# Performance work log

Measured on AMD Instinct MI355X. Metric: run time of the kernel, lower is better.

The kernel has to match this reference:

```python
import jax, jax.numpy as jnp
import numpy as np

N_NODES = 100000
N_EDGES = 1600000
H_IN = 128
H_OUT = 128
ELU_ALPHA = 0.1


def setup_inputs() -> dict:
    key = jax.random.key(0)
    k = jax.random.split(key, 6)
    x = jax.random.normal(k[0], (N_NODES, H_IN), dtype=jnp.float32)
    edge_index = jax.random.randint(k[1], (2, N_EDGES), 0, N_NODES, dtype=jnp.int64)
    s = 1.0 / np.sqrt(H_IN)
    W_conv = jax.random.uniform(k[2], (H_IN, H_OUT), jnp.float32, -s, s)
    b_conv = jnp.zeros((H_OUT,), jnp.float32)
    W_skip = jax.random.uniform(k[3], (H_IN, H_OUT), jnp.float32, -s, s)
    b_skip = jax.random.uniform(k[4], (H_OUT,), jnp.float32, -s, s)
    return {"x": x, "edge_index": edge_index, "W_conv": W_conv,
            "b_conv": b_conv, "W_skip": W_skip, "b_skip": b_skip}


def reference(x, edge_index, W_conv, b_conv, W_skip, b_skip):
    # GCNConv(improved=True): add self-loops with weight 2.0, symmetric norm.
    N = x.shape[0]
    src, dst = edge_index[0], edge_index[1]
    # degree = incoming edge weights (1.0 each) + 2.0 self-loop weight
    deg = jnp.zeros((N,), x.dtype).at[dst].add(1.0) + 2.0
    dinv = jax.lax.rsqrt(deg)                     # deg >= 2 always
    norm = dinv[src] * dinv[dst]                  # [E]
    h = x @ W_conv                                # [N, H_OUT]
    # scatter-add of normalized messages over real edges
    agg = jax.ops.segment_sum(norm[:, None] * h[src], dst, num_segments=N)
    # self-loop contribution: weight 2 * dinv[i]^2
    agg = agg + (2.0 * dinv * dinv)[:, None] * h
    out = agg + b_conv + x @ W_skip + b_skip
    # Dropout(p=0.1) in eval mode = identity; ELU(alpha=0.1)
    return jnp.where(out > 0, out, ELU_ALPHA * (jnp.exp(out) - 1.0))
```

## Files before the change

### kernel.cpp

```cpp
#include <hip/hip_runtime.h>
#include <hip/hip_bf16.h>
#include <hip/hip_fp16.h>

#define H 128
#define BW 128
#define BSH 7
#define NB 256
#define TK 32

typedef __attribute__((ext_vector_type(8))) short short8;
typedef __attribute__((ext_vector_type(4))) float f32x4;

__device__ inline unsigned short f2bf(float f) {
    union { float f; unsigned int u; } v; v.f = f;
    unsigned int r = (v.u + 0x7fffu + ((v.u >> 16) & 1u)) >> 16;
    return (unsigned short)r;
}
__device__ inline float bf2f(unsigned short h) {
    union { unsigned int u; float f; } v; v.u = ((unsigned int)h) << 16;
    return v.f;
}

__global__ __launch_bounds__(256) void quant_hist_kernel(const float* __restrict__ x,
                                                         const float* __restrict__ Wc,
                                                         const float* __restrict__ Ws,
                                                         const int* __restrict__ ei,
                                                         uint* __restrict__ xq,
                                                         float* __restrict__ invs,
                                                         short8* __restrict__ wp,
                                                         int* __restrict__ counts,
                                                         int N, int E, int nbu,
                                                         int chunk, int qb) {
    __shared__ int h[1024];
    if (blockIdx.x >= qb) {
        const int b = blockIdx.x - qb;
        for (int i = threadIdx.x; i < nbu; i += 256) h[i] = 0;
        __syncthreads();
        const int lo = b * chunk;
        const int hi = min(E, lo + chunk);
        for (int e = lo + threadIdx.x; e < hi; e += 256)
            atomicAdd(&h[ei[E + e] >> BSH], 1);
        __syncthreads();
        for (int i = threadIdx.x; i < nbu; i += 256) counts[b * nbu + i] = h[i];
        return;
    }
    int node = blockIdx.x * 8 + (threadIdx.x >> 5);
    if (node < N) {
        int l32 = threadIdx.x & 31;
        float4 v = ((const float4*)x)[node * 32 + l32];
        float m = fmaxf(fmaxf(fabsf(v.x), fabsf(v.y)), fmaxf(fabsf(v.z), fabsf(v.w)));
        #pragma unroll
        for (int mk = 1; mk < 32; mk <<= 1) m = fmaxf(m, __shfl_xor(m, mk));
        m = fmaxf(m, 1e-30f);
        float s = 127.0f / m;
        int q0 = min(255, max(0, (int)rintf(v.x * s) + 128));
        int q1 = min(255, max(0, (int)rintf(v.y * s) + 128));
        int q2 = min(255, max(0, (int)rintf(v.z * s) + 128));
        int q3 = min(255, max(0, (int)rintf(v.w * s) + 128));
        xq[node * 32 + l32] = (uint)q0 | ((uint)q1 << 8) | ((uint)q2 << 16) | ((uint)q3 << 24);
        if (l32 == 0) invs[node] = m / 127.0f;
    }
    if (blockIdx.x < 8) {
        int t = blockIdx.x * 256 + threadIdx.x;
        int lane = t & 63;
        int nt = (t >> 6) & 7;
        int ks = t >> 9;
        int kbase = ks * 32 + (lane >> 4) * 8;
        int col = nt * 16 + (lane & 15);
        short8 whc, whs, wls;
        #pragma unroll
        for (int j = 0; j < 8; ++j) {
            float wc = Wc[(kbase + j) * H + col];
            float ws = Ws[(kbase + j) * H + col];
            unsigned short hc = f2bf(wc);
            unsigned short hs = f2bf(ws);
            whc[j] = (short)hc;
            whs[j] = (short)hs;
            wls[j] = (short)f2bf(ws - bf2f(hs));
        }
        int base = (ks * 8 + nt) * 64 + lane;
        wp[base] = whc;
        wp[2048 + base] = whs;
        wp[4096 + base] = wls;
    }
}

__global__ __launch_bounds__(256) void p2_scan(const int* __restrict__ counts,
                                               int* __restrict__ scanned,
                                               int* __restrict__ btot, int nbu) {
    __shared__ int tile[NB][TK + 1];
    __shared__ int segsum[8][TK + 1];
    const int tl = threadIdx.x & 31;
    const int tw = threadIdx.x >> 5;
    const int k = blockIdx.x * TK + tl;
    const bool kok = k < nbu;
    for (int r = tw; r < NB; r += 8)
        tile[r][tl] = kok ? counts[r * nbu + k] : 0;
    __syncthreads();
    const int base = tw * 32;
    int s = 0;
    #pragma unroll
    for (int i = 0; i < 32; ++i) s += tile[base + i][tl];
    segsum[tw][tl] = s;
    __syncthreads();
    int run = 0;
    for (int q = 0; q < tw; ++q) run += segsum[q][tl];
    if (kok) {
        for (int i = 0; i < 32; ++i) {
            int cur = tile[base + i][tl];
            scanned[(base + i) * nbu + k] = run;
            run += cur;
        }
        if (tw == 7) btot[k] = run;
    }
}

__global__ __launch_bounds__(256) void p5_scatter(const int* __restrict__ ei,
                                                  const int* __restrict__ btot,
                                                  const int* __restrict__ scanned,
                                                  int* __restrict__ tmp,
                                                  int* __restrict__ cstart,
                                                  int E, int nbu, int chunk) {
    __shared__ int sc[1024];
    __shared__ int part[256];
    __shared__ int lb[1024];
    const int t = threadIdx.x;
    const int b = blockIdx.x;
    const int base = t * 4;
    int v0 = (base + 0 < nbu) ? btot[base + 0] : 0;
    int v1 = (base + 1 < nbu) ? btot[base + 1] : 0;
    int v2 = (base + 2 < nbu) ? btot[base + 2] : 0;
    int v3 = (base + 3 < nbu) ? btot[base + 3] : 0;
    int s1 = v0 + v1, s2 = s1 + v2, s3 = s2 + v3;
    part[t] = s3;
    __syncthreads();
    for (int off = 1; off < 256; off <<= 1) {
        int a = (t >= off) ? part[t - off] : 0;
        __syncthreads();
        part[t] += a;
        __syncthreads();
    }
    int add = (t > 0) ? part[t - 1] : 0;
    sc[base + 0] = add;
    sc[base + 1] = add + v0;
    sc[base + 2] = add + s1;
    sc[base + 3] = add + s2;
    __syncthreads();
    if (b == 0) {
        for (int k = t; k < nbu; k += 256) cstart[k] = sc[k];
        if (t == 0) cstart[nbu] = E;
    }
    for (int k = t; k < nbu; k += 256) lb[k] = sc[k] + scanned[b * nbu + k];
    __syncthreads();
    const int lo = b * chunk;
    const int hi = min(E, lo + chunk);
    for (int e = lo + t; e < hi; e += 256) {
        int s = ei[e], d = ei[E + e];
        int slot = atomicAdd(&lb[d >> BSH], 1);
        tmp[slot] = ((d & (BW - 1)) << 17) | s;
    }
}

__global__ __launch_bounds__(256) void csr_kernel(const int* __restrict__ tmp,
                                                  const int* __restrict__ cstart,
                                                  const float* __restrict__ invs,
                                                  int* __restrict__ entries,
                                                  int* __restrict__ rstart,
                                                  float* __restrict__ dinv,
                                                  float* __restrict__ ainv,
                                                  float* __restrict__ selfw,
                                                  int N, int E) {
    __shared__ int ldeg[BW];
    __shared__ int lscan[BW];
    __shared__ int lcur[BW];
    const int b = blockIdx.x;
    const int nstart = b << BSH;
    const int estart = cstart[b];
    const int eend = cstart[b + 1];
    const int t = threadIdx.x;

    if (t < BW) ldeg[t] = 0;
    __syncthreads();
    for (int i = estart + t; i < eend; i += 256)
        atomicAdd(&ldeg[(tmp[i] >> 17) & (BW - 1)], 1);
    __syncthreads();
    if (t < BW) lscan[t] = ldeg[t];
    __syncthreads();
    #pragma unroll
    for (int off = 1; off < BW; off <<= 1) {
        int a = 0;
        if (t < BW && t >= off) a = lscan[t - off];
        __syncthreads();
        if (t < BW) lscan[t] += a;
        __syncthreads();
    }
    if (t < BW) {
        int excl = lscan[t] - ldeg[t];
        lcur[t] = excl;
        int n = nstart + t;
        if (n < N) {
            float iv = invs[n];
            float dv = rsqrtf((float)ldeg[t] + 2.0f);
            rstart[n] = estart + excl;
            dinv[n] = dv;
            ainv[n] = dv * iv;
            selfw[n] = 2.0f * dv * dv * iv;
        }
    }
    __syncthreads();
    for (int i = estart + t; i < eend; i += 256) {
        int v = tmp[i];
        int sl = atomicAdd(&lcur[(v >> 17) & (BW - 1)], 1);
        entries[estart + sl] = v & 0x1FFFF;
    }
    if (b == 0 && t == 0) rstart[N] = E;
}

__global__ __launch_bounds__(256) void agg_kernel(const int* __restrict__ entries,
                                                  const int* __restrict__ rstart,
                                                  const float* __restrict__ dinv,
                                                  const float* __restrict__ ainv,
                                                  const float* __restrict__ selfw,
                                                  const uint* __restrict__ xq,
                                                  unsigned short* __restrict__ z, int N) {
    int node = blockIdx.x * 16 + (threadIdx.x >> 4);
    if (node >= N) return;
    const int l16 = threadIdx.x & 15;
    const uint2* x2 = (const uint2*)xq;

    int start = rstart[node];
    int end = rstart[node + 1];
    float dd = dinv[node];
    float sw = selfw[node];
    uint2 qs = x2[node * 16 + l16];

    float a0 = 0.f, a1 = 0.f, a2 = 0.f, a3 = 0.f;
    float a4 = 0.f, a5 = 0.f, a6 = 0.f, a7 = 0.f;
    float sumw = 0.f;

    for (int c = start; c < end; c += 16) {
        int rem = end - c;
        int src = 0;
        float w = 0.f;
        if (l16 < rem) {
            src = entries[c + l16];
            w = ainv[src] * dd;
        }
        #pragma unroll 4
        for (int j = 0; j < 16; ++j) {
            int ss = __shfl(src, j, 16);
            float wv = __shfl(w, j, 16);
            if (wv != 0.f) {
                uint2 q = x2[ss * 16 + l16];
                sumw += wv;
                a0 += wv * (float)(q.x & 0xffu);
                a1 += wv * (float)((q.x >> 8) & 0xffu);
                a2 += wv * (float)((q.x >> 16) & 0xffu);
                a3 += wv * (float)(q.x >> 24);
                a4 += wv * (float)(q.y & 0xffu);
                a5 += wv * (float)((q.y >> 8) & 0xffu);
                a6 += wv * (float)((q.y >> 16) & 0xffu);
                a7 += wv * (float)(q.y >> 24);
            }
        }
    }

    sumw += sw;
    a0 += sw * (float)(qs.x & 0xffu);
    a1 += sw * (float)((qs.x >> 8) & 0xffu);
    a2 += sw * (float)((qs.x >> 16) & 0xffu);
    a3 += sw * (float)(qs.x >> 24);
    a4 += sw * (float)(qs.y & 0xffu);
    a5 += sw * (float)((qs.y >> 8) & 0xffu);
    a6 += sw * (float)((qs.y >> 16) & 0xffu);
    a7 += sw * (float)(qs.y >> 24);

    float off = 128.f * sumw;
    uint4 o;
    o.x = (uint)f2bf(a0 - off) | ((uint)f2bf(a1 - off) << 16);
    o.y = (uint)f2bf(a2 - off) | ((uint)f2bf(a3 - off) << 16);
    o.z = (uint)f2bf(a4 - off) | ((uint)f2bf(a5 - off) << 16);
    o.w = (uint)f2bf(a6 - off) | ((uint)f2bf(a7 - off) << 16);
    ((uint4*)z)[node * 16 + l16] = o;
}

__global__ __launch_bounds__(256) void gemm_kernel(const unsigned short* __restrict__ zb,
                                                   const float* __restrict__ x,
                                                   const short8* __restrict__ wp,
                                                   const float* __restrict__ bc,
                                                   const float* __restrict__ bsk,
                                                   float* __restrict__ out, int N) {
    __shared__ short8 bsm[1536];
    const int tid = threadIdx.x;
    const int lane = tid & 63;
    const int wave = tid >> 6;
    const int m = lane & 15;
    const int quad = lane >> 4;
    const int row = blockIdx.x * 64 + wave * 16 + m;
    const bool rowok = row < N;

    f32x4 acc[8];
    #pragma unroll
    for (int i = 0; i < 8; ++i) acc[i] = (f32x4){0.f, 0.f, 0.f, 0.f};

    #pragma unroll
    for (int ks = 0; ks < 4; ++ks) {
        const int k0 = ks * 32 + quad * 8;
        short8 za = {0, 0, 0, 0, 0, 0, 0, 0};
        short8 xa_h = {0, 0, 0, 0, 0, 0, 0, 0};
        short8 xa_l = {0, 0, 0, 0, 0, 0, 0, 0};
        if (rowok) {
            za = ((const short8*)zb)[(row * H + k0) >> 3];
            float4 a = *(const float4*)&x[row * H + k0];
            float4 b = *(const float4*)&x[row * H + k0 + 4];
            float xv[8] = {a.x, a.y, a.z, a.w, b.x, b.y, b.z, b.w};
            #pragma unroll
            for (int j = 0; j < 8; ++j) {
                unsigned short h = f2bf(xv[j]);
                xa_h[j] = (short)h;
                xa_l[j] = (short)f2bf(xv[j] - bf2f(h));
            }
        }
        __syncthreads();
        #pragma unroll
        for (int p = 0; p < 3; ++p) {
            bsm[p * 512 + tid]       = wp[p * 2048 + ks * 512 + tid];
            bsm[p * 512 + 256 + tid] = wp[p * 2048 + ks * 512 + 256 + tid];
        }
        __syncthreads();
        #pragma unroll
        for (int nt = 0; nt < 8; ++nt) {
            short8 bch = bsm[nt * 64 + lane];
            short8 bsh = bsm[512 + nt * 64 + lane];
            short8 bsl = bsm[1024 + nt * 64 + lane];
            acc[nt] = __builtin_amdgcn_mfma_f32_16x16x32_bf16(za, bch, acc[nt], 0, 0, 0);
            acc[nt] = __builtin_amdgcn_mfma_f32_16x16x32_bf16(xa_h, bsh, acc[nt], 0, 0, 0);
            acc[nt] = __builtin_amdgcn_mfma_f32_16x16x32_bf16(xa_l, bsh, acc[nt], 0, 0, 0);
            acc[nt] = __builtin_amdgcn_mfma_f32_16x16x32_bf16(xa_h, bsl, acc[nt], 0, 0, 0);
        }
    }

    const int orow_base = blockIdx.x * 64 + wave * 16 + quad * 4;
    #pragma unroll
    for (int nt = 0; nt < 8; ++nt) {
        int col = nt * 16 + m;
        float bias = bc[col] + bsk[col];
        #pragma unroll
        for (int r = 0; r < 4; ++r) {
            int orow = orow_base + r;
            if (orow < N) {
                float v = acc[nt][r] + bias;
                v = v > 0.f ? v : 0.1f * (__expf(v) - 1.f);
                out[orow * H + col] = v;
            }
        }
    }
}

extern "C" void kernel_launch(void* const* d_in, const int* in_sizes, int n_in,
                              void* d_out, int out_size, void* d_ws, size_t ws_size,
                              hipStream_t stream) {
    const float* x   = (const float*)d_in[0];
    const int*   ei  = (const int*)d_in[1];
    const float* Wc  = (const float*)d_in[2];
    const float* bc  = (const float*)d_in[3];
    const float* Wsk = (const float*)d_in[4];
    const float* bsk = (const float*)d_in[5];
    float* out = (float*)d_out;

    const int N = in_sizes[0] / H;
    const int E = in_sizes[1] / 2;
    const int nbu = (N + BW - 1) / BW;
    const int chunk = (E + NB - 1) / NB;
    const int qb = (N + 7) / 8;

    char* w = (char*)d_ws;
    short8*         wp      = (short8*)w;
    int*            rstart  = (int*)(w + 131072);
    float*          dinv    = (float*)(w + 540672);
    float*          ainv    = (float*)(w + 942080);
    float*          selfw   = (float*)(w + 1343488);
    int*            entries = (int*)(w + 1744896);
    uint*           xq      = (uint*)(w + 8146944);
    unsigned short* z       = (unsigned short*)(w + 20971520);
    float*          invs    = (float*)(w + 20971520);
    int*            cstart  = (int*)(w + 21371520);
    int*            btot    = (int*)(w + 21374784);
    int*            counts  = (int*)(w + 21377984);
    int*            scanned = (int*)(w + 22178752);
    int*            tmp     = (int*)(w + 22979520);

    quant_hist_kernel<<<qb + NB, 256, 0, stream>>>(x, Wc, Wsk, ei, xq, invs, wp,
                                                   counts, N, E, nbu, chunk, qb);

    p2_scan<<<(nbu + TK - 1) / TK, 256, 0, stream>>>(counts, scanned, btot, nbu);

    p5_scatter<<<NB, 256, 0, stream>>>(ei, btot, scanned, tmp, cstart, E, nbu, chunk);

    csr_kernel<<<nbu, 256, 0, stream>>>(tmp, cstart, invs, entries, rstart,
                                        dinv, ainv, selfw, N, E);

    agg_kernel<<<(N + 15) / 16, 256, 0, stream>>>(entries, rstart, dinv, ainv,
                                                  selfw, xq, z, N);

    gemm_kernel<<<(N + 63) / 64, 256, 0, stream>>>(z, x, wp, bc, bsk, out, N);
}
```

Before: 251.1 us.

## Fuse neighbor aggregation into GEMM kernel via swizzled shared-memory staging

```diff
diff --git a/kernel.cpp b/kernel.cpp
--- a/kernel.cpp
+++ b/kernel.cpp
@@ -216,88 +216,94 @@
     if (b == 0 && t == 0) rstart[N] = E;
 }
 
-__global__ __launch_bounds__(256) void agg_kernel(const int* __restrict__ entries,
-                                                  const int* __restrict__ rstart,
-                                                  const float* __restrict__ dinv,
-                                                  const float* __restrict__ ainv,
-                                                  const float* __restrict__ selfw,
-                                                  const uint* __restrict__ xq,
-                                                  unsigned short* __restrict__ z, int N) {
-    int node = blockIdx.x * 16 + (threadIdx.x >> 4);
-    if (node >= N) return;
-    const int l16 = threadIdx.x & 15;
-    const uint2* x2 = (const uint2*)xq;
-
-    int start = rstart[node];
-    int end = rstart[node + 1];
-    float dd = dinv[node];
-    float sw = selfw[node];
-    uint2 qs = x2[node * 16 + l16];
-
-    float a0 = 0.f, a1 = 0.f, a2 = 0.f, a3 = 0.f;
-    float a4 = 0.f, a5 = 0.f, a6 = 0.f, a7 = 0.f;
-    float sumw = 0.f;
-
-    for (int c = start; c < end; c += 16) {
-        int rem = end - c;
-        int src = 0;
-        float w = 0.f;
-        if (l16 < rem) {
-            src = entries[c + l16];
-            w = ainv[src] * dd;
-        }
-        #pragma unroll 4
-        for (int j = 0; j < 16; ++j) {
-            int ss = __shfl(src, j, 16);
-            float wv = __shfl(w, j, 16);
-            if (wv != 0.f) {
-                uint2 q = x2[ss * 16 + l16];
-                sumw += wv;
-                a0 += wv * (float)(q.x & 0xffu);
-                a1 += wv * (float)((q.x >> 8) & 0xffu);
-                a2 += wv * (float)((q.x >> 16) & 0xffu);
-                a3 += wv * (float)(q.x >> 24);
-                a4 += wv * (float)(q.y & 0xffu);
-                a5 += wv * (float)((q.y >> 8) & 0xffu);
-                a6 += wv * (float)((q.y >> 16) & 0xffu);
-                a7 += wv * (float)(q.y >> 24);
-            }
-        }
-    }
-
-    sumw += sw;
-    a0 += sw * (float)(qs.x & 0xffu);
-    a1 += sw * (float)((qs.x >> 8) & 0xffu);
-    a2 += sw * (float)((qs.x >> 16) & 0xffu);
-    a3 += sw * (float)(qs.x >> 24);
-    a4 += sw * (float)(qs.y & 0xffu);
-    a5 += sw * (float)((qs.y >> 8) & 0xffu);
-    a6 += sw * (float)((qs.y >> 16) & 0xffu);
-    a7 += sw * (float)(qs.y >> 24);
-
-    float off = 128.f * sumw;
-    uint4 o;
-    o.x = (uint)f2bf(a0 - off) | ((uint)f2bf(a1 - off) << 16);
-    o.y = (uint)f2bf(a2 - off) | ((uint)f2bf(a3 - off) << 16);
-    o.z = (uint)f2bf(a4 - off) | ((uint)f2bf(a5 - off) << 16);
-    o.w = (uint)f2bf(a6 - off) | ((uint)f2bf(a7 - off) << 16);
-    ((uint4*)z)[node * 16 + l16] = o;
-}
-
-__global__ __launch_bounds__(256) void gemm_kernel(const unsigned short* __restrict__ zb,
-                                                   const float* __restrict__ x,
-                                                   const short8* __restrict__ wp,
-                                                   const float* __restrict__ bc,
-                                                   const float* __restrict__ bsk,
-                                                   float* __restrict__ out, int N) {
+__global__ __launch_bounds__(256) void agg_gemm_kernel(const int* __restrict__ entries,
+                                                       const int* __restrict__ rstart,
+                                                       const float* __restrict__ dinv,
+                                                       const float* __restrict__ ainv,
+                                                       const float* __restrict__ selfw,
+                                                       const uint* __restrict__ xq,
+                                                       const float* __restrict__ x,
+                                                       const short8* __restrict__ wp,
+                                                       const float* __restrict__ bc,
+                                                       const float* __restrict__ bsk,
+                                                       float* __restrict__ out, int N) {
+    __shared__ uint zs[4096];
     __shared__ short8 bsm[1536];
     const int tid = threadIdx.x;
+    const int l16 = tid & 15;
+    const int qid = tid >> 4;
+    const uint2* x2 = (const uint2*)xq;
+
+    #pragma unroll 1
+    for (int rep = 0; rep < 4; ++rep) {
+        const int zrow = rep * 16 + qid;
+        const int node = blockIdx.x * 64 + zrow;
+        if (node < N) {
+            int start = rstart[node];
+            int end = rstart[node + 1];
+            float dd = dinv[node];
+            float sw = selfw[node];
+            uint2 qs = x2[node * 16 + l16];
+
+            float a0 = 0.f, a1 = 0.f, a2 = 0.f, a3 = 0.f;
+            float a4 = 0.f, a5 = 0.f, a6 = 0.f, a7 = 0.f;
+            float sumw = 0.f;
+
+            for (int c = start; c < end; c += 16) {
+                int rem = end - c;
+                int src = 0;
+                float w = 0.f;
+                if (l16 < rem) {
+                    src = entries[c + l16];
+                    w = ainv[src] * dd;
+                }
+                #pragma unroll 4
+                for (int j = 0; j < 16; ++j) {
+                    int ss = __shfl(src, j, 16);
+                    float wv = __shfl(w, j, 16);
+                    if (wv != 0.f) {
+                        uint2 q = x2[ss * 16 + l16];
+                        sumw += wv;
+                        a0 += wv * (float)(q.x & 0xffu);
+                        a1 += wv * (float)((q.x >> 8) & 0xffu);
+                        a2 += wv * (float)((q.x >> 16) & 0xffu);
+                        a3 += wv * (float)(q.x >> 24);
+                        a4 += wv * (float)(q.y & 0xffu);
+                        a5 += wv * (float)((q.y >> 8) & 0xffu);
+                        a6 += wv * (float)((q.y >> 16) & 0xffu);
+                        a7 += wv * (float)(q.y >> 24);
+                    }
+                }
+            }
+
+            sumw += sw;
+            a0 += sw * (float)(qs.x & 0xffu);
+            a1 += sw * (float)((qs.x >> 8) & 0xffu);
+            a2 += sw * (float)((qs.x >> 16) & 0xffu);
+            a3 += sw * (float)(qs.x >> 24);
+            a4 += sw * (float)(qs.y & 0xffu);
+            a5 += sw * (float)((qs.y >> 8) & 0xffu);
+            a6 += sw * (float)((qs.y >> 16) & 0xffu);
+            a7 += sw * (float)(qs.y >> 24);
+
+            float off = 128.f * sumw;
+            uint4 o;
+            o.x = (uint)f2bf(a0 - off) | ((uint)f2bf(a1 - off) << 16);
+            o.y = (uint)f2bf(a2 - off) | ((uint)f2bf(a3 - off) << 16);
+            o.z = (uint)f2bf(a4 - off) | ((uint)f2bf(a5 - off) << 16);
+            o.w = (uint)f2bf(a6 - off) | ((uint)f2bf(a7 - off) << 16);
+            *(uint4*)&zs[zrow * 64 + ((l16 * 4) ^ ((zrow & 7) * 4))] = o;
+        }
+    }
+    __syncthreads();
+
     const int lane = tid & 63;
     const int wave = tid >> 6;
     const int m = lane & 15;
     const int quad = lane >> 4;
     const int row = blockIdx.x * 64 + wave * 16 + m;
     const bool rowok = row < N;
+    const int zr = wave * 16 + m;
 
     f32x4 acc[8];
     #pragma unroll
@@ -306,11 +312,10 @@
     #pragma unroll
     for (int ks = 0; ks < 4; ++ks) {
         const int k0 = ks * 32 + quad * 8;
-        short8 za = {0, 0, 0, 0, 0, 0, 0, 0};
+        short8 za = *(const short8*)&zs[zr * 64 + ((ks * 16 + quad * 4) ^ ((zr & 7) * 4))];
         short8 xa_h = {0, 0, 0, 0, 0, 0, 0, 0};
         short8 xa_l = {0, 0, 0, 0, 0, 0, 0, 0};
         if (rowok) {
-            za = ((const short8*)zb)[(row * H + k0) >> 3];
             float4 a = *(const float4*)&x[row * H + k0];
             float4 b = *(const float4*)&x[row * H + k0 + 4];
             float xv[8] = {a.x, a.y, a.z, a.w, b.x, b.y, b.z, b.w};
@@ -382,7 +387,6 @@
     float*          selfw   = (float*)(w + 1343488);
     int*            entries = (int*)(w + 1744896);
     uint*           xq      = (uint*)(w + 8146944);
-    unsigned short* z       = (unsigned short*)(w + 20971520);
     float*          invs    = (float*)(w + 20971520);
     int*            cstart  = (int*)(w + 21371520);
     int*            btot    = (int*)(w + 21374784);
@@ -400,8 +404,7 @@
     csr_kernel<<<nbu, 256, 0, stream>>>(tmp, cstart, invs, entries, rstart,
                                         dinv, ainv, selfw, N, E);
 
-    agg_kernel<<<(N + 15) / 16, 256, 0, stream>>>(entries, rstart, dinv, ainv,
-                                                  selfw, xq, z, N);
-
-    gemm_kernel<<<(N + 63) / 64, 256, 0, stream>>>(z, x, wp, bc, bsk, out, N);
-}
+    agg_gemm_kernel<<<(N + 63) / 64, 256, 0, stream>>>(entries, rstart, dinv, ainv,
+                                                       selfw, xq, x, wp, bc, bsk,
+                                                       out, N);
+}
```

New measurement: 285.1 us. +13.5%, slower.
